# Kernel tuning notes

Hardware: AMD Instinct MI355X
Metric: run time of the kernel (lower is better)

Reference implementation:

```python
import jax, jax.numpy as jnp
import numpy as np

NUM_HEADS = 4
LN_EPS = 1e-5


def setup_inputs() -> dict:
    key = jax.random.key(0)
    ks = jax.random.split(key, 12)
    B, S, D = 8, 2048, 256
    Dh = D // NUM_HEADS
    s = 0.02
    return {
        "descriptors": jax.random.normal(ks[0], (B, S, D), jnp.float32),
        # cached rotary embedding (cos, sin) pair broadcastable over heads
        "keypoints": jax.random.normal(ks[1], (2, B, 1, S, Dh), jnp.float32),
        "Wqkv_w": jax.random.normal(ks[2], (3 * D, D), jnp.float32) * s,
        "Wqkv_b": jax.random.normal(ks[3], (3 * D,), jnp.float32) * s,
        "Wo_w": jax.random.normal(ks[4], (D, D), jnp.float32) * s,
        "Wo_b": jax.random.normal(ks[5], (D,), jnp.float32) * s,
        "W1_w": jax.random.normal(ks[6], (2 * D, 2 * D), jnp.float32) * s,
        "W1_b": jax.random.normal(ks[7], (2 * D,), jnp.float32) * s,
        "ln_g": jnp.ones((2 * D,), jnp.float32),
        "ln_b": jnp.zeros((2 * D,), jnp.float32),
        "W2_w": jax.random.normal(ks[8], (D, 2 * D), jnp.float32) * s,
        "W2_b": jax.random.normal(ks[9], (D,), jnp.float32) * s,
    }


def _rotate_half(x):
    # pairwise rotation: (x0,x1,x2,x3,...) -> (-x1,x0,-x3,x2,...)
    xr = x.reshape(x.shape[:-1] + (x.shape[-1] // 2, 2))
    return jnp.stack((-xr[..., 1], xr[..., 0]), axis=-1).reshape(x.shape)


def reference(descriptors, keypoints, Wqkv_w, Wqkv_b, Wo_w, Wo_b,
              W1_w, W1_b, ln_g, ln_b, W2_w, W2_b):
    B, S, D = descriptors.shape
    H = NUM_HEADS
    Dh = D // H
    # fused QKV projection; torch layout: last dim = (H, Dh, 3) interleaved
    qkv = descriptors @ Wqkv_w.T + Wqkv_b           # [B,S,3D]
    qkv = qkv.reshape(B, S, H, Dh, 3).transpose(0, 2, 1, 3, 4)  # [B,H,S,Dh,3]
    q, k, v = qkv[..., 0], qkv[..., 1], qkv[..., 2]
    # rotary embedding on q, k
    cos, sin = keypoints[0], keypoints[1]           # [B,1,S,Dh]
    q = q * cos + _rotate_half(q) * sin
    k = k * cos + _rotate_half(k) * sin
    # scaled dot-product attention
    scale = jnp.float32(Dh) ** -0.5
    sim = jnp.einsum('bhid,bhjd->bhij', q, k) * scale
    attn = jax.nn.softmax(sim, axis=-1)
    ctx = jnp.einsum('bhij,bhjd->bhid', attn, v)    # [B,H,S,Dh]
    ctx = ctx.transpose(0, 2, 1, 3).reshape(B, S, D)
    message = ctx @ Wo_w.T + Wo_b
    # FFN over concat(descriptors, message)
    x = jnp.concatenate([descriptors, message], axis=-1)  # [B,S,2D]
    x = x @ W1_w.T + W1_b
    mu = jnp.mean(x, axis=-1, keepdims=True)
    var = jnp.var(x, axis=-1, keepdims=True)
    x = (x - mu) * jax.lax.rsqrt(var + LN_EPS) * ln_g + ln_b
    x = jax.nn.gelu(x, approximate=False)
    x = x @ W2_w.T + W2_b
    return descriptors + x
```

## Files before the change

kernel.cpp:

```cpp
#include <hip/hip_runtime.h>
#include <math.h>

#define B_  8
#define S_  2048
#define D_  256
#define H_  4
#define DH  64
#define M_  (B_ * S_)
#define QS  4194304

typedef __attribute__((ext_vector_type(8))) short bf16x8;
typedef __attribute__((ext_vector_type(4))) float f32x4;
typedef unsigned short u16;
typedef unsigned int   u32;

#define AS1 __attribute__((address_space(1)))
#define AS3 __attribute__((address_space(3)))

__device__ __forceinline__ u16 f2bf(float x) {
    union { float f; u32 u; } c; c.f = x;
    u32 r = (c.u + 0x7fffu + ((c.u >> 16) & 1u)) >> 16;
    return (u16)r;
}
__device__ __forceinline__ float bf2f(u16 x) {
    union { u32 u; float f; } c; c.u = ((u32)x) << 16;
    return c.f;
}

__device__ __forceinline__ void gload16(const void* g, void* l) {
    __builtin_amdgcn_global_load_lds((const AS1 unsigned int*)g,
                                     (AS3 unsigned int*)l, 16, 0, 0);
}

__global__ __launch_bounds__(256) void cast5_kernel(
    const float* __restrict__ s0, u16* __restrict__ d0,
    const float* __restrict__ s1, u16* __restrict__ d1,
    const float* __restrict__ s2, u16* __restrict__ d2,
    const float* __restrict__ s3, u16* __restrict__ d3,
    const float* __restrict__ s4, u16* __restrict__ d4)
{
    int bid = blockIdx.x;
    const float* s; u16* d;
    if      (bid < 4096) { s = s0; d = d0; }
    else if (bid < 4288) { s = s1; d = d1; bid -= 4096; }
    else if (bid < 4352) { s = s2; d = d2; bid -= 4288; }
    else if (bid < 4608) { s = s3; d = d3; bid -= 4352; }
    else                 { s = s4; d = d4; bid -= 4608; }
    const int i = (bid * 256 + threadIdx.x) * 4;
    const float4 v = *(const float4*)(s + i);
    u16 o[4] = {f2bf(v.x), f2bf(v.y), f2bf(v.z), f2bf(v.w)};
    *(uint2*)(d + i) = *(const uint2*)o;
}

template <int NT, int CONCAT, int RES, int OUTBF16>
__global__ __launch_bounds__(256) void gemm_bf16(
    const u16* __restrict__ A, const u16* __restrict__ A2,
    const u16* __restrict__ W, const float* __restrict__ bias,
    const float* __restrict__ res, float* __restrict__ Cf,
    u16* __restrict__ Cb, int K, int N)
{
    __shared__ u16 As[128 * 64];
    __shared__ u16 Bs[NT * 32 * 64];
    const int tid  = threadIdx.x;
    const int w    = tid >> 6;
    const int lane = tid & 63;
    const int n    = lane & 15;
    const int quad = lane >> 4;
    const int m0   = blockIdx.x * 128;
    const int n0   = blockIdx.y * (NT * 32);
    const int m_off = (w >> 1) * 64;
    const int n_off = (w & 1) * (NT * 16);
    const int lrow = lane >> 3;
    const int lcol = (lane & 7) * 8;

    f32x4 acc[4][NT];
#pragma unroll
    for (int i = 0; i < 4; i++)
#pragma unroll
        for (int j = 0; j < NT; j++) acc[i][j] = (f32x4){0.f, 0.f, 0.f, 0.f};

    for (int k0 = 0; k0 < K; k0 += 64) {
        const u16* Asrc;
        int kb, lda;
        if (CONCAT) { Asrc = (k0 < 256) ? A : A2; kb = k0 & 255; lda = 256; }
        else        { Asrc = A; kb = k0; lda = K; }

        __syncthreads();
#pragma unroll
        for (int it = 0; it < 4; it++) {
            const int r0 = it * 32 + w * 8;
            gload16(Asrc + (size_t)(m0 + r0 + lrow) * lda + kb + lcol, &As[r0 * 64]);
        }
#pragma unroll
        for (int it = 0; it < NT; it++) {
            const int r0 = it * 32 + w * 8;
            gload16(W + (size_t)(n0 + r0 + lrow) * K + k0 + lcol, &Bs[r0 * 64]);
        }
        __syncthreads();

        bf16x8 af[4][2], bf[NT][2];
#pragma unroll
        for (int mt = 0; mt < 4; mt++)
#pragma unroll
            for (int t = 0; t < 2; t++)
                af[mt][t] = *(const bf16x8*)&As[(m_off + mt * 16 + n) * 64 + t * 32 + quad * 8];
#pragma unroll
        for (int nt = 0; nt < NT; nt++)
#pragma unroll
            for (int t = 0; t < 2; t++)
                bf[nt][t] = *(const bf16x8*)&Bs[(n_off + nt * 16 + n) * 64 + t * 32 + quad * 8];

#pragma unroll
        for (int mt = 0; mt < 4; mt++)
#pragma unroll
            for (int nt = 0; nt < NT; nt++) {
                acc[mt][nt] = __builtin_amdgcn_mfma_f32_16x16x32_bf16(af[mt][0], bf[nt][0], acc[mt][nt], 0, 0, 0);
                acc[mt][nt] = __builtin_amdgcn_mfma_f32_16x16x32_bf16(af[mt][1], bf[nt][1], acc[mt][nt], 0, 0, 0);
            }
    }

#pragma unroll
    for (int nt = 0; nt < NT; nt++) {
        const int col = n0 + n_off + nt * 16 + n;
        const float bv = bias[col];
#pragma unroll
        for (int mt = 0; mt < 4; mt++) {
#pragma unroll
            for (int r = 0; r < 4; r++) {
                const int row = m0 + m_off + mt * 16 + quad * 4 + r;
                float o = acc[mt][nt][r] + bv;
                if (RES) o += res[(size_t)row * N + col];
                if (OUTBF16) Cb[(size_t)row * N + col] = f2bf(o);
                else         Cf[(size_t)row * N + col] = o;
            }
        }
    }
}

__global__ __launch_bounds__(256) void rope_kernel(
    const u16* __restrict__ qkv, const float* __restrict__ kp,
    u16* __restrict__ q, u16* __restrict__ k, u16* __restrict__ v)
{
    const int row = blockIdx.x * 2 + (threadIdx.x >> 7);
    const int t   = threadIdx.x & 127;
    const int b   = row >> 11;
    const int s   = row & 2047;
    const int h   = t >> 5;
    const int dp  = t & 31;
    const int d   = dp * 2;

    const u16* src = qkv + (size_t)row * 768 + h * 192 + dp * 6;
    const u32 w0 = *(const u32*)(src);
    const u32 w1 = *(const u32*)(src + 2);
    const u32 w2 = *(const u32*)(src + 4);
    const float qe = bf2f((u16)w0), ke = bf2f((u16)(w0 >> 16));
    const float qo = bf2f((u16)(w1 >> 16));
    const float ko = bf2f((u16)w2);

    const size_t kidx = ((size_t)b * S_ + s) * DH + d;
    const float2 cs = *(const float2*)(kp + kidx);
    const float2 sn = *(const float2*)(kp + (size_t)B_ * S_ * DH + kidx);

    const float qe2 = (qe * cs.x - qo * sn.x) * 0.125f;
    const float qo2 = (qo * cs.y + qe * sn.y) * 0.125f;
    const float ke2 = ke * cs.x - ko * sn.x;
    const float ko2 = ko * cs.y + ke * sn.y;

    const size_t oidx = (((size_t)(b * H_ + h)) * S_ + s) * DH + d;
    *(u32*)(q + oidx) = (u32)f2bf(qe2) | ((u32)f2bf(qo2) << 16);
    *(u32*)(k + oidx) = (u32)f2bf(ke2) | ((u32)f2bf(ko2) << 16);
    *(u32*)(v + oidx) = (w1 & 0xffffu) | (w2 & 0xffff0000u);
}

__global__ __launch_bounds__(256) void vtrans_kernel(
    const u16* __restrict__ v, u16* __restrict__ vt)
{
    const int bh = blockIdx.x;
    const int s  = blockIdx.y * 256 + threadIdx.x;
    const u16* src = v + ((size_t)bh * S_ + s) * DH;
    u16* dst = vt + (size_t)bh * DH * S_ + s;
#pragma unroll
    for (int g = 0; g < 8; g++) {
        const uint4 vv = *(const uint4*)(src + g * 8);
        const u16* us = (const u16*)&vv;
#pragma unroll
        for (int i = 0; i < 8; i++) dst[(size_t)(g * 8 + i) * S_] = us[i];
    }
}

__global__ __launch_bounds__(256, 2) void attn_kernel(
    const u16* __restrict__ q, const u16* __restrict__ k,
    const u16* __restrict__ vt, u16* __restrict__ ctx)
{
    __shared__ u16 pool[3 * 8192];
    u16* ks = pool;
    u16* qs = pool + 8192;
    u16* vs = pool + 16384;

    const int tid  = threadIdx.x;
    const int w    = tid >> 6;
    const int lane = tid & 63;
    const int n    = lane & 15;
    const int quad = lane >> 4;
    const int lrow = lane >> 3;
    const int vrow = lane >> 4;
    const int bh   = blockIdx.x;
    const int q0   = blockIdx.y * 128;
    const int b    = bh >> 2;
    const int h    = bh & 3;
    const int nsw  = n & 7;

    const int kcol  = (((lane & 7) ^ lrow) * 8);
    const int vcol0 = (((lane & 15) ^ vrow) * 8);
    const int vcol1 = (((lane & 15) ^ (4 + vrow)) * 8);

    const u16* qbase = q  + (size_t)bh * S_ * DH;
    const u16* kbase = k  + (size_t)bh * S_ * DH;
    const u16* vbase = vt + (size_t)bh * DH * S_;

#pragma unroll
    for (int it = 0; it < 4; it++) {
        const int idx = it * 256 + tid;
        const int row = idx >> 3;
        const int c8  = idx & 7;
        *(uint4*)&qs[row * 64 + ((c8 ^ (row & 7)) * 8)] =
            *(const uint4*)(qbase + (size_t)(q0 + row) * DH + c8 * 8);
    }
    __syncthreads();

    bf16x8 qf[2][2];
#pragma unroll
    for (int mb = 0; mb < 2; mb++) {
        qf[mb][0] = *(const bf16x8*)&qs[(w * 32 + mb * 16 + n) * 64 + ((quad       ^ nsw) * 8)];
        qf[mb][1] = *(const bf16x8*)&qs[(w * 32 + mb * 16 + n) * 64 + (((4 + quad) ^ nsw) * 8)];
    }

    f32x4 o[2][4];
#pragma unroll
    for (int mb = 0; mb < 2; mb++)
#pragma unroll
        for (int j = 0; j < 4; j++) o[mb][j] = (f32x4){0.f, 0.f, 0.f, 0.f};
    float lrun[2][4] = {{0.f, 0.f, 0.f, 0.f}, {0.f, 0.f, 0.f, 0.f}};

    for (int kb = 0; kb < S_ / 128; kb++) {
        const int k0 = kb * 128;
        __syncthreads();
#pragma unroll
        for (int it = 0; it < 4; it++) {
            const int r0 = w * 32 + it * 8;
            gload16(kbase + (size_t)(k0 + r0 + lrow) * DH + kcol, &ks[r0 * 64]);
            const int d0 = w * 16 + it * 4;
            gload16(vbase + (size_t)(d0 + vrow) * S_ + k0 + ((it & 1) ? vcol1 : vcol0),
                    &vs[d0 * 128]);
        }
        __syncthreads();

        f32x4 sacc[2][8];
#pragma unroll
        for (int mb = 0; mb < 2; mb++)
#pragma unroll
            for (int j = 0; j < 8; j++)
                sacc[mb][j] = (f32x4){-12.f, -12.f, -12.f, -12.f};
#pragma unroll
        for (int t = 0; t < 2; t++) {
#pragma unroll
            for (int j = 0; j < 8; j++) {
                const bf16x8 kf = *(const bf16x8*)
                    &ks[(16 * j + n) * 64 + (((t * 4 + quad) ^ nsw) * 8)];
                sacc[0][j] = __builtin_amdgcn_mfma_f32_16x16x32_bf16(qf[0][t], kf, sacc[0][j], 0, 0, 0);
                sacc[1][j] = __builtin_amdgcn_mfma_f32_16x16x32_bf16(qf[1][t], kf, sacc[1][j], 0, 0, 0);
            }
        }
        __syncthreads();

#pragma unroll
        for (int mb = 0; mb < 2; mb++) {
#pragma unroll
            for (int r = 0; r < 4; r++) {
                float rs = 0.f;
                const int rw8  = (quad * 4 + r) & 7;
                const int prow = (w * 32 + mb * 16 + quad * 4 + r) * 128;
#pragma unroll
                for (int j = 0; j < 8; j++) {
                    const float p = __expf(sacc[mb][j][r]);
                    rs += p;
                    pool[prow + (((2 * j + (n >> 3)) ^ rw8) * 8) + (n & 7)] = f2bf(p);
                }
                lrun[mb][r] += rs;
            }
        }

#pragma unroll
        for (int kt = 0; kt < 4; kt++) {
            const bf16x8 pf0 = *(const bf16x8*)
                &pool[(w * 32 +      n) * 128 + (((kt * 4 + quad) ^ nsw) * 8)];
            const bf16x8 pf1 = *(const bf16x8*)
                &pool[(w * 32 + 16 + n) * 128 + (((kt * 4 + quad) ^ nsw) * 8)];
#pragma unroll
            for (int nt = 0; nt < 4; nt++) {
                const bf16x8 vf = *(const bf16x8*)
                    &vs[(16 * nt + n) * 128 + (((kt * 4 + quad) ^ nsw) * 8)];
                o[0][nt] = __builtin_amdgcn_mfma_f32_16x16x32_bf16(pf0, vf, o[0][nt], 0, 0, 0);
                o[1][nt] = __builtin_amdgcn_mfma_f32_16x16x32_bf16(pf1, vf, o[1][nt], 0, 0, 0);
            }
        }
    }

#pragma unroll
    for (int mb = 0; mb < 2; mb++) {
#pragma unroll
        for (int r = 0; r < 4; r++) {
            float s = lrun[mb][r];
            s += __shfl_xor(s, 1);
            s += __shfl_xor(s, 2);
            s += __shfl_xor(s, 4);
            s += __shfl_xor(s, 8);
            lrun[mb][r] = s;
        }
    }

#pragma unroll
    for (int mb = 0; mb < 2; mb++) {
#pragma unroll
        for (int r = 0; r < 4; r++) {
            const float inv = 1.f / lrun[mb][r];
            const int row = q0 + w * 32 + mb * 16 + quad * 4 + r;
#pragma unroll
            for (int nt = 0; nt < 4; nt++)
                ctx[((size_t)b * S_ + row) * D_ + h * DH + 16 * nt + n] = f2bf(o[mb][nt][r] * inv);
        }
    }
}

__global__ __launch_bounds__(256) void ln_gelu_kernel(
    const float* __restrict__ x, const float* __restrict__ g,
    const float* __restrict__ bt, u16* __restrict__ y)
{
    __shared__ float ss[4], sqs[4];
    const int m = blockIdx.x;
    const float* row = x + (size_t)m * 512;
    const int t = threadIdx.x;
    const float v0 = row[t];
    const float v1 = row[t + 256];
    float s  = v0 + v1;
    float sq = v0 * v0 + v1 * v1;
#pragma unroll
    for (int off = 1; off < 64; off <<= 1) {
        s  += __shfl_xor(s, off);
        sq += __shfl_xor(sq, off);
    }
    const int w = t >> 6;
    if ((t & 63) == 0) { ss[w] = s; sqs[w] = sq; }
    __syncthreads();
    s  = ss[0] + ss[1] + ss[2] + ss[3];
    sq = sqs[0] + sqs[1] + sqs[2] + sqs[3];
    const float mu   = s * (1.f / 512.f);
    const float var  = sq * (1.f / 512.f) - mu * mu;
    const float rstd = rsqrtf(var + 1e-5f);

    const float y0 = (v0 - mu) * rstd * g[t] + bt[t];
    const float y1 = (v1 - mu) * rstd * g[t + 256] + bt[t + 256];
    y[(size_t)m * 512 + t]       = f2bf(0.5f * y0 * (1.f + erff(y0 * 0.70710678118654752f)));
    y[(size_t)m * 512 + t + 256] = f2bf(0.5f * y1 * (1.f + erff(y1 * 0.70710678118654752f)));
}

extern "C" void kernel_launch(void* const* d_in, const int* in_sizes, int n_in,
                              void* d_out, int out_size, void* d_ws, size_t ws_size,
                              hipStream_t stream)
{
    const float* desc   = (const float*)d_in[0];
    const float* kp     = (const float*)d_in[1];
    const float* Wqkv_w = (const float*)d_in[2];
    const float* Wqkv_b = (const float*)d_in[3];
    const float* Wo_w   = (const float*)d_in[4];
    const float* Wo_b   = (const float*)d_in[5];
    const float* W1_w   = (const float*)d_in[6];
    const float* W1_b   = (const float*)d_in[7];
    const float* ln_g   = (const float*)d_in[8];
    const float* ln_b   = (const float*)d_in[9];
    const float* W2_w   = (const float*)d_in[10];
    const float* W2_b   = (const float*)d_in[11];
    float* out = (float*)d_out;
    float* ws  = (float*)d_ws;

    u16*   qkvb  = (u16*)ws;
    float* x1    = ws;
    u16*   x1b   = (u16*)(ws + 2 * (size_t)QS);
    u16*   qb    = (u16*)(ws + 3 * (size_t)QS);
    u16*   kb    = (u16*)(ws + (size_t)(3.5 * QS));
    u16*   vb    = (u16*)(ws + 4 * (size_t)QS);
    u16*   ctxb  = (u16*)(ws + (size_t)(4.5 * QS));
    u16*   descb = (u16*)(ws + 5 * (size_t)QS);
    u16*   msgb  = (u16*)(ws + (size_t)(5.5 * QS));
    u16*   wpool = (u16*)(ws + 6 * (size_t)QS);
    u16*   vtb   = (u16*)(ws + (size_t)(6.5 * QS));
    u16* wqkvb = wpool;
    u16* wob   = wqkvb + 196608;
    u16* w1b   = wob   + 65536;
    u16* w2b   = w1b   + 262144;

    const dim3 blk(256);

    cast5_kernel<<<dim3(4736), blk, 0, stream>>>(
        desc, descb, Wqkv_w, wqkvb, Wo_w, wob, W1_w, w1b, W2_w, w2b);

    gemm_bf16<4, 0, 0, 1><<<dim3(M_ / 128, 768 / 128), blk, 0, stream>>>(
        descb, nullptr, wqkvb, Wqkv_b, nullptr, nullptr, qkvb, 256, 768);

    rope_kernel<<<dim3(M_ / 2), blk, 0, stream>>>(qkvb, kp, qb, kb, vb);

    vtrans_kernel<<<dim3(B_ * H_, S_ / 256), blk, 0, stream>>>(vb, vtb);

    attn_kernel<<<dim3(B_ * H_, S_ / 128), blk, 0, stream>>>(qb, kb, vtb, ctxb);

    gemm_bf16<2, 0, 0, 1><<<dim3(M_ / 128, 256 / 64), blk, 0, stream>>>(
        ctxb, nullptr, wob, Wo_b, nullptr, nullptr, msgb, 256, 256);

    gemm_bf16<4, 1, 0, 0><<<dim3(M_ / 128, 512 / 128), blk, 0, stream>>>(
        descb, msgb, w1b, W1_b, nullptr, x1, nullptr, 512, 512);

    ln_gelu_kernel<<<dim3(M_), blk, 0, stream>>>(x1, ln_g, ln_b, x1b);

    gemm_bf16<2, 0, 1, 0><<<dim3(M_ / 128, 256 / 64), blk, 0, stream>>>(
        x1b, nullptr, w2b, W2_b, desc, out, nullptr, 512, 256);
}
```

Baseline: 245.5 us.

## Transpose QK^T MFMA so each lane owns a query row and packs P stores

The QK^T MFMA operands are swapped so the score tile comes out transposed: each lane holds four consecutive key columns for a single query row. This lets the softmax exponentials be packed into 8-byte LDS stores with a new XOR swizzle, and it reduces the row-sum reduction to a few shuffles done once at the end. P gets its own shared buffer instead of aliasing the K/Q/V pool, which removes one __syncthreads per key block. The cost is more LDS per block (80 KB vs 48 KB), which could reduce occupancy below the requested two blocks per CU.

```diff
diff --git a/kernel.cpp b/kernel.cpp
--- a/kernel.cpp
+++ b/kernel.cpp
@@ -192,10 +192,10 @@
     const u16* __restrict__ q, const u16* __restrict__ k,
     const u16* __restrict__ vt, u16* __restrict__ ctx)
 {
-    __shared__ u16 pool[3 * 8192];
-    u16* ks = pool;
-    u16* qs = pool + 8192;
-    u16* vs = pool + 16384;
+    __shared__ u16 ks[128 * 64];
+    __shared__ u16 qs[128 * 64];
+    __shared__ u16 vs[64 * 128];
+    __shared__ u16 ps[128 * 128];
 
     const int tid  = threadIdx.x;
     const int w    = tid >> 6;
@@ -240,7 +240,7 @@
     for (int mb = 0; mb < 2; mb++)
 #pragma unroll
         for (int j = 0; j < 4; j++) o[mb][j] = (f32x4){0.f, 0.f, 0.f, 0.f};
-    float lrun[2][4] = {{0.f, 0.f, 0.f, 0.f}, {0.f, 0.f, 0.f, 0.f}};
+    float lrun[2] = {0.f, 0.f};
 
     for (int kb = 0; kb < S_ / 128; kb++) {
         const int k0 = kb * 128;
@@ -267,35 +267,37 @@
             for (int j = 0; j < 8; j++) {
                 const bf16x8 kf = *(const bf16x8*)
                     &ks[(16 * j + n) * 64 + (((t * 4 + quad) ^ nsw) * 8)];
-                sacc[0][j] = __builtin_amdgcn_mfma_f32_16x16x32_bf16(qf[0][t], kf, sacc[0][j], 0, 0, 0);
-                sacc[1][j] = __builtin_amdgcn_mfma_f32_16x16x32_bf16(qf[1][t], kf, sacc[1][j], 0, 0, 0);
+                sacc[0][j] = __builtin_amdgcn_mfma_f32_16x16x32_bf16(kf, qf[0][t], sacc[0][j], 0, 0, 0);
+                sacc[1][j] = __builtin_amdgcn_mfma_f32_16x16x32_bf16(kf, qf[1][t], sacc[1][j], 0, 0, 0);
             }
         }
-        __syncthreads();
 
 #pragma unroll
         for (int mb = 0; mb < 2; mb++) {
-#pragma unroll
-            for (int r = 0; r < 4; r++) {
-                float rs = 0.f;
-                const int rw8  = (quad * 4 + r) & 7;
-                const int prow = (w * 32 + mb * 16 + quad * 4 + r) * 128;
-#pragma unroll
-                for (int j = 0; j < 8; j++) {
-                    const float p = __expf(sacc[mb][j][r]);
-                    rs += p;
-                    pool[prow + (((2 * j + (n >> 3)) ^ rw8) * 8) + (n & 7)] = f2bf(p);
-                }
-                lrun[mb][r] += rs;
+            float rs = 0.f;
+            const int prow = (w * 32 + mb * 16 + n) * 128;
+#pragma unroll
+            for (int j = 0; j < 8; j++) {
+                const float e0 = __expf(sacc[mb][j][0]);
+                const float e1 = __expf(sacc[mb][j][1]);
+                const float e2 = __expf(sacc[mb][j][2]);
+                const float e3 = __expf(sacc[mb][j][3]);
+                rs += (e0 + e1) + (e2 + e3);
+                uint2 pk;
+                pk.x = (u32)f2bf(e0) | ((u32)f2bf(e1) << 16);
+                pk.y = (u32)f2bf(e2) | ((u32)f2bf(e3) << 16);
+                const int blk = (4 * j + quad) ^ (nsw << 2);
+                *(uint2*)&ps[prow + blk * 4] = pk;
             }
+            lrun[mb] += rs;
         }
 
 #pragma unroll
         for (int kt = 0; kt < 4; kt++) {
             const bf16x8 pf0 = *(const bf16x8*)
-                &pool[(w * 32 +      n) * 128 + (((kt * 4 + quad) ^ nsw) * 8)];
+                &ps[(w * 32 +      n) * 128 + ((32 * kt + 8 * quad) ^ (nsw << 4))];
             const bf16x8 pf1 = *(const bf16x8*)
-                &pool[(w * 32 + 16 + n) * 128 + (((kt * 4 + quad) ^ nsw) * 8)];
+                &ps[(w * 32 + 16 + n) * 128 + ((32 * kt + 8 * quad) ^ (nsw << 4))];
 #pragma unroll
             for (int nt = 0; nt < 4; nt++) {
                 const bf16x8 vf = *(const bf16x8*)
@@ -308,22 +310,18 @@
 
 #pragma unroll
     for (int mb = 0; mb < 2; mb++) {
+        float s = lrun[mb];
+        s += __shfl_xor(s, 16);
+        s += __shfl_xor(s, 32);
+        lrun[mb] = s;
+    }
+
+#pragma unroll
+    for (int mb = 0; mb < 2; mb++) {
 #pragma unroll
         for (int r = 0; r < 4; r++) {
-            float s = lrun[mb][r];
-            s += __shfl_xor(s, 1);
-            s += __shfl_xor(s, 2);
-            s += __shfl_xor(s, 4);
-            s += __shfl_xor(s, 8);
-            lrun[mb][r] = s;
-        }
-    }
-
-#pragma unroll
-    for (int mb = 0; mb < 2; mb++) {
-#pragma unroll
-        for (int r = 0; r < 4; r++) {
-            const float inv = 1.f / lrun[mb][r];
+            const float sv = __shfl(lrun[mb], quad * 4 + r);
+            const float inv = 1.f / sv;
             const int row = q0 + w * 32 + mb * 16 + quad * 4 + r;
 #pragma unroll
             for (int nt = 0; nt < 4; nt++)
```

Result: no change. 245.2 us (-0.1%).
